# Performance work log

Hardware: AMD Instinct MI355X
Metric: run time of the kernel (lower is better)

Reference implementation:

```python
import jax, jax.numpy as jnp
import numpy as np

B, S, D, H = 2, 2048, 1024, 16
HD = D // H  # head_dim = 64


def setup_inputs() -> dict:
    key = jax.random.key(0)
    ks = jax.random.split(key, 10)
    sc = 1.0 / np.sqrt(D)
    x = jax.random.normal(ks[0], (B, S, D), dtype=jnp.float32)
    # causal mask, 0 = masked (module does masked_fill(mask == 0, -1e9))
    mask = jnp.broadcast_to(jnp.tril(jnp.ones((S, S), dtype=jnp.int32)), (B, S, S))
    return {
        "x": x,
        "mask": mask,
        "Wq": jax.random.normal(ks[1], (D, D), dtype=jnp.float32) * sc,
        "bq": jnp.zeros((D,), dtype=jnp.float32),
        "Wk": jax.random.normal(ks[2], (D, D), dtype=jnp.float32) * sc,
        "bk": jnp.zeros((D,), dtype=jnp.float32),
        "Wv": jax.random.normal(ks[3], (D, D), dtype=jnp.float32) * sc,
        "bv": jnp.zeros((D,), dtype=jnp.float32),
        "Wo": jax.random.normal(ks[4], (D, D), dtype=jnp.float32) * sc,
        "bo": jnp.zeros((D,), dtype=jnp.float32),
    }


def reference(x, mask, Wq, bq, Wk, bk, Wv, bv, Wo, bo):
    b, s, _ = x.shape
    # torch nn.Linear: y = x @ W.T + b
    def split_heads(t):
        return t.reshape(b, s, H, HD).transpose(0, 2, 1, 3)  # [B,H,S,hd]
    q = split_heads(x @ Wq.T + bq)
    k = split_heads(x @ Wk.T + bk)
    v = split_heads(x @ Wv.T + bv)
    scores = jnp.einsum("bhqd,bhkd->bhqk", q, k) / jnp.sqrt(jnp.float32(HD))
    scores = jnp.where(mask[:, None, :, :] == 0, jnp.float32(-1e9), scores)
    w = jax.nn.softmax(scores, axis=-1)
    out = jnp.einsum("bhqk,bhkd->bhqd", w, v)  # [B,H,S,hd]
    out = out.transpose(0, 2, 1, 3).reshape(b, s, D)
    return out @ Wo.T + bo
```

## Files before the change

kernel.cpp:

```cpp
#include <hip/hip_runtime.h>
#include <cstdint>


typedef __bf16 bf16x8 __attribute__((ext_vector_type(8)));
typedef float f32x4 __attribute__((ext_vector_type(4)));

__device__ inline f32x4 mfma16(bf16x8 a, bf16x8 b, f32x4 c) {
    return __builtin_amdgcn_mfma_f32_16x16x32_bf16(a, b, c, 0, 0, 0);
}

__device__ inline uint16_t f2bf(float f) {
    uint32_t u = __builtin_bit_cast(uint32_t, f);
    u += 0x7FFFu + ((u >> 16) & 1u);
    return (uint16_t)(u >> 16);
}

__device__ inline void gload_lds16(const uint16_t* g, uint16_t* l) {
    __builtin_amdgcn_global_load_lds(
        (const __attribute__((address_space(1))) uint32_t*)g,
        (__attribute__((address_space(3))) uint32_t*)l, 16, 0, 0);
}

__global__ __launch_bounds__(256) void cast_kernel(const float* __restrict__ src,
                                                   uint16_t* __restrict__ dst, int n4) {
    int i = blockIdx.x * 256 + threadIdx.x;
    if (i < n4) {
        float4 v = ((const float4*)src)[i];
        uint64_t p = (uint64_t)f2bf(v.x) | ((uint64_t)f2bf(v.y) << 16) |
                     ((uint64_t)f2bf(v.z) << 32) | ((uint64_t)f2bf(v.w) << 48);
        ((uint64_t*)dst)[i] = p;
    }
}

__global__ __launch_bounds__(256) void cast4_kernel(const float* __restrict__ a,
                                                    const float* __restrict__ b,
                                                    const float* __restrict__ c,
                                                    const float* __restrict__ d,
                                                    uint16_t* __restrict__ dst, int n4) {
    const float* srcs[4] = {a, b, c, d};
    const float* s = srcs[blockIdx.y];
    int i = blockIdx.x * 256 + threadIdx.x;
    if (i < n4) {
        float4 v = ((const float4*)s)[i];
        uint64_t p = (uint64_t)f2bf(v.x) | ((uint64_t)f2bf(v.y) << 16) |
                     ((uint64_t)f2bf(v.z) << 32) | ((uint64_t)f2bf(v.w) << 48);
        ((uint64_t*)(dst + (size_t)blockIdx.y * n4 * 4))[i] = p;
    }
}

template<int OUTF32>
__global__ __launch_bounds__(256) void gemm128(const uint16_t* __restrict__ A,
                                               const uint16_t* __restrict__ W,
                                               const float* __restrict__ b0,
                                               const float* __restrict__ b1,
                                               const float* __restrict__ b2,
                                               void* __restrict__ o0,
                                               void* __restrict__ o1,
                                               void* __restrict__ o2,
                                               int K, float s0, float s1, float s2) {
    __shared__ __align__(16) uint16_t Alds[2][128 * 32];
    __shared__ __align__(16) uint16_t Blds[2][128 * 32];
    const int tid = threadIdx.x;
    const int lane = tid & 63, w = tid >> 6;
    const int l16 = lane & 15, quad = lane >> 4;
    const int wm = w & 1, wn = w >> 1;
    const int m0 = blockIdx.x * 128, n0 = blockIdx.y * 128;

    f32x4 acc[4][4] = {};

    const int ci0 = w * 128 + lane;
    const uint16_t* ga0 = A + (size_t)(m0 + (ci0 >> 2)) * K + (ci0 & 3) * 8;
    const uint16_t* gb0 = W + (size_t)(n0 + (ci0 >> 2)) * K + (ci0 & 3) * 8;
    const int ci1 = ci0 + 64;
    const uint16_t* ga1 = A + (size_t)(m0 + (ci1 >> 2)) * K + (ci1 & 3) * 8;
    const uint16_t* gb1 = W + (size_t)(n0 + (ci1 >> 2)) * K + (ci1 & 3) * 8;

    gload_lds16(ga0, Alds[0] + (w * 2 + 0) * 512);
    gload_lds16(gb0, Blds[0] + (w * 2 + 0) * 512);
    gload_lds16(ga1, Alds[0] + (w * 2 + 1) * 512);
    gload_lds16(gb1, Blds[0] + (w * 2 + 1) * 512);

    const int niter = K >> 5;
    for (int i = 0; i < niter; ++i) {
        __syncthreads();
        if (i + 1 < niter) {
            const int k1 = (i + 1) << 5;
            uint16_t* Ad = Alds[(i + 1) & 1];
            uint16_t* Bd = Blds[(i + 1) & 1];
            gload_lds16(ga0 + k1, Ad + (w * 2 + 0) * 512);
            gload_lds16(gb0 + k1, Bd + (w * 2 + 0) * 512);
            gload_lds16(ga1 + k1, Ad + (w * 2 + 1) * 512);
            gload_lds16(gb1 + k1, Bd + (w * 2 + 1) * 512);
        }
        const uint16_t* Ab = Alds[i & 1];
        const uint16_t* Bb = Blds[i & 1];
        bf16x8 af[4], bw[4];
#pragma unroll
        for (int t = 0; t < 4; ++t) {
            af[t] = *(const bf16x8*)(Ab + (wm * 64 + t * 16 + l16) * 32 + quad * 8);
            bw[t] = *(const bf16x8*)(Bb + (wn * 64 + t * 16 + l16) * 32 + quad * 8);
        }
#pragma unroll
        for (int mt = 0; mt < 4; ++mt)
#pragma unroll
            for (int nt = 0; nt < 4; ++nt)
                acc[mt][nt] = mfma16(af[mt], bw[nt], acc[mt][nt]);
    }

#pragma unroll
    for (int nt = 0; nt < 4; ++nt) {
        int col = n0 + wn * 64 + nt * 16 + l16;
        int seg = col >> 10, lcol = col & 1023;
        const float* bp = (seg == 0) ? b0 : (seg == 1 ? b1 : b2);
        float scale    = (seg == 0) ? s0 : (seg == 1 ? s1 : s2);
        void* op       = (seg == 0) ? o0 : (seg == 1 ? o1 : o2);
        float bc = bp[lcol];
#pragma unroll
        for (int mt = 0; mt < 4; ++mt)
#pragma unroll
            for (int r = 0; r < 4; ++r) {
                int row = m0 + wm * 64 + mt * 16 + quad * 4 + r;
                float v = (acc[mt][nt][r] + bc) * scale;
                if (OUTF32) ((float*)op)[(size_t)row * 1024 + lcol] = v;
                else        ((uint16_t*)op)[(size_t)row * 1024 + lcol] = f2bf(v);
            }
    }
}

__global__ __launch_bounds__(256) void transpose_v(const uint16_t* __restrict__ V,
                                                   uint16_t* __restrict__ Vt) {
    __shared__ __align__(16) uint16_t T[64 * 72];
    const int s0 = blockIdx.x * 64;
    const int bh = blockIdx.y;
    const int b = bh >> 4, h = bh & 15;
    const int tid = threadIdx.x;
    const int r = tid >> 2, c = tid & 3;
#pragma unroll
    for (int half = 0; half < 2; ++half) {
        uint4 v = *(const uint4*)(V + (size_t)(b * 2048 + s0 + r) * 1024 + h * 64 + half * 32 + c * 8);
        *(uint4*)(T + r * 72 + half * 32 + c * 8) = v;
    }
    __syncthreads();
#pragma unroll
    for (int it = 0; it < 2; ++it) {
        int id = it * 256 + tid;
        int d = id >> 3, c8 = (id & 7) * 8;
        uint32_t wpk[4];
#pragma unroll
        for (int jj = 0; jj < 4; ++jj) {
            uint32_t lo = T[(c8 + 2 * jj) * 72 + d];
            uint32_t hi = T[(c8 + 2 * jj + 1) * 72 + d];
            wpk[jj] = lo | (hi << 16);
        }
        uint4 o; o.x = wpk[0]; o.y = wpk[1]; o.z = wpk[2]; o.w = wpk[3];
        *(uint4*)(Vt + ((size_t)bh * 64 + d) * 2048 + s0 + c8) = o;
    }
}

__global__ __launch_bounds__(256) void attn_kernel(const uint16_t* __restrict__ Q,
                                                   const uint16_t* __restrict__ K,
                                                   const uint16_t* __restrict__ Vt,
                                                   float* __restrict__ Oacc,
                                                   float* __restrict__ Lbuf) {
    const int S = 2048, D = 1024;
    __shared__ __align__(16) uint16_t Klds[64 * 72];
    __shared__ __align__(16) uint16_t Vlds[64 * 72];
    __shared__ __align__(16) uint16_t Plds[4 * 32 * 72];

    int x = 39 - (int)blockIdx.x;
    int g = (x >= 24) ? 3 : (x >= 12) ? 2 : (x >= 4) ? 1 : 0;
    int rem = x - 2 * g * (g + 1);
    int per = g + 1;
    int qb = 4 * g + rem / per;
    int chunk = rem % per;
    const int n_kb = 2 * qb + 2, kb_diag = 2 * qb;
    const int kb0 = chunk * 8;
    const int kb1 = (kb0 + 8 < n_kb) ? kb0 + 8 : n_kb;
    const int niter = kb1 - kb0;

    const int bh = blockIdx.y;
    const int b = bh >> 4, h = bh & 15;
    const int tid = threadIdx.x, lane = tid & 63, w = tid >> 6;
    const int l16 = lane & 15, quad = lane >> 4;
    const int q0 = qb * 128;
    const size_t baseQK = (size_t)b * S * D + h * 64;
    uint16_t* Pw = Plds + w * (32 * 72);

    bf16x8 aq[2][2];
#pragma unroll
    for (int mt = 0; mt < 2; ++mt)
#pragma unroll
        for (int c = 0; c < 2; ++c)
            aq[mt][c] = *(const bf16x8*)(Q + baseQK +
                (size_t)(q0 + w * 32 + mt * 16 + l16) * D + c * 32 + quad * 8);

    bf16x8 ones;
#pragma unroll
    for (int j = 0; j < 8; ++j) ones[j] = (__bf16)1.0f;

    f32x4 accO[2][4] = {};
    f32x4 accL[2] = {};

    const int srow = tid >> 2, scq = tid & 3;
    const uint16_t* Kg = K + baseQK + (size_t)srow * D + scq * 16;
    const uint16_t* Vg = Vt + ((size_t)bh * 64 + srow) * S + scq * 16;

    uint4 kA, kB, vA, vB;
    {
        const uint16_t* kg = Kg + (size_t)(kb0 * 64) * D;
        const uint16_t* vg = Vg + kb0 * 64;
        kA = *(const uint4*)kg; kB = *(const uint4*)(kg + 8);
        vA = *(const uint4*)vg; vB = *(const uint4*)(vg + 8);
    }

    for (int i = 0; i < niter; ++i) {
        const int kb = kb0 + i;
        if (i) __syncthreads();
        *(uint4*)(Klds + srow * 72 + scq * 16)     = kA;
        *(uint4*)(Klds + srow * 72 + scq * 16 + 8) = kB;
        *(uint4*)(Vlds + srow * 72 + scq * 16)     = vA;
        *(uint4*)(Vlds + srow * 72 + scq * 16 + 8) = vB;
        if (i + 1 < niter) {
            const uint16_t* kg = Kg + (size_t)((kb + 1) * 64) * D;
            const uint16_t* vg = Vg + (kb + 1) * 64;
            kA = *(const uint4*)kg; kB = *(const uint4*)(kg + 8);
            vA = *(const uint4*)vg; vB = *(const uint4*)(vg + 8);
        }
        __syncthreads();

        f32x4 sc[2][4];
#pragma unroll
        for (int t = 0; t < 4; ++t) {
            bf16x8 bk0 = *(const bf16x8*)(Klds + (t * 16 + l16) * 72 + quad * 8);
            bf16x8 bk1 = *(const bf16x8*)(Klds + (t * 16 + l16) * 72 + 32 + quad * 8);
            f32x4 z0 = {}; f32x4 z1 = {};
            sc[0][t] = mfma16(aq[0][1], bk1, mfma16(aq[0][0], bk0, z0));
            sc[1][t] = mfma16(aq[1][1], bk1, mfma16(aq[1][0], bk0, z1));
        }

        bf16x8 bv0[4], bv1[4];
#pragma unroll
        for (int nt = 0; nt < 4; ++nt) {
            bv0[nt] = *(const bf16x8*)(Vlds + (nt * 16 + l16) * 72 + quad * 8);
            bv1[nt] = *(const bf16x8*)(Vlds + (nt * 16 + l16) * 72 + 32 + quad * 8);
        }

        if (kb < kb_diag) {
#pragma unroll
            for (int mt = 0; mt < 2; ++mt)
#pragma unroll
                for (int r = 0; r < 4; ++r)
#pragma unroll
                    for (int t = 0; t < 4; ++t) {
                        float p = __builtin_amdgcn_exp2f(sc[mt][t][r]);
                        Pw[(mt * 16 + quad * 4 + r) * 72 + t * 16 + l16] =
                            (uint16_t)(__builtin_bit_cast(uint32_t, p) >> 16);
                    }
        } else {
#pragma unroll
            for (int mt = 0; mt < 2; ++mt)
#pragma unroll
                for (int r = 0; r < 4; ++r) {
                    const int qrow = q0 + w * 32 + mt * 16 + quad * 4 + r;
#pragma unroll
                    for (int t = 0; t < 4; ++t) {
                        float s = sc[mt][t][r];
                        int kcol = kb * 64 + t * 16 + l16;
                        if (kcol > qrow) s = -1e30f;
                        float p = __builtin_amdgcn_exp2f(s);
                        Pw[(mt * 16 + quad * 4 + r) * 72 + t * 16 + l16] =
                            (uint16_t)(__builtin_bit_cast(uint32_t, p) >> 16);
                    }
                }
        }

        __asm__ volatile("s_waitcnt lgkmcnt(0)" ::: "memory");

        bf16x8 ap0[2], ap1[2];
#pragma unroll
        for (int mt = 0; mt < 2; ++mt) {
            ap0[mt] = *(const bf16x8*)(Pw + (mt * 16 + l16) * 72 + quad * 8);
            ap1[mt] = *(const bf16x8*)(Pw + (mt * 16 + l16) * 72 + 32 + quad * 8);
        }
#pragma unroll
        for (int nt = 0; nt < 4; ++nt) {
            accO[0][nt] = mfma16(ap1[0], bv1[nt], mfma16(ap0[0], bv0[nt], accO[0][nt]));
            accO[1][nt] = mfma16(ap1[1], bv1[nt], mfma16(ap0[1], bv0[nt], accO[1][nt]));
        }
        accL[0] = mfma16(ap1[0], ones, mfma16(ap0[0], ones, accL[0]));
        accL[1] = mfma16(ap1[1], ones, mfma16(ap0[1], ones, accL[1]));
    }

#pragma unroll
    for (int mt = 0; mt < 2; ++mt)
#pragma unroll
        for (int r = 0; r < 4; ++r) {
            const int qrow = q0 + w * 32 + mt * 16 + quad * 4 + r;
            const size_t rh = (size_t)(b * S + qrow) * 16 + h;
            if (l16 == 0) atomicAdd(Lbuf + rh, accL[mt][r]);
            float* ob = Oacc + rh * 64 + l16;
#pragma unroll
            for (int nt = 0; nt < 4; ++nt)
                atomicAdd(ob + nt * 16, accO[mt][nt][r]);
        }
}

__global__ __launch_bounds__(256) void norm_kernel(const float* __restrict__ Oacc,
                                                   const float* __restrict__ Lbuf,
                                                   uint16_t* __restrict__ att) {
    int idx = blockIdx.x * 256 + threadIdx.x;
    float4 o = ((const float4*)Oacc)[idx];
    float inv = __builtin_amdgcn_rcpf(Lbuf[idx >> 4]);
    uint64_t p = (uint64_t)f2bf(o.x * inv) | ((uint64_t)f2bf(o.y * inv) << 16) |
                 ((uint64_t)f2bf(o.z * inv) << 32) | ((uint64_t)f2bf(o.w * inv) << 48);
    ((uint64_t*)att)[idx] = p;
}

extern "C" void kernel_launch(void* const* d_in, const int* in_sizes, int n_in,
                              void* d_out, int out_size, void* d_ws, size_t ws_size,
                              hipStream_t stream) {
    const float* x  = (const float*)d_in[0];
    const float* Wq = (const float*)d_in[2];
    const float* bq = (const float*)d_in[3];
    const float* Wk = (const float*)d_in[4];
    const float* bk = (const float*)d_in[5];
    const float* Wv = (const float*)d_in[6];
    const float* bv = (const float*)d_in[7];
    const float* Wo = (const float*)d_in[8];
    const float* bo = (const float*)d_in[9];
    float* out = (float*)d_out;

    const int B = 2, S = 2048, D = 1024, H = 16;
    const int M = B * S;

    uint8_t* w = (uint8_t*)d_ws;
    uint16_t* xbf  = (uint16_t*)(w);
    uint16_t* wqbf = (uint16_t*)(w + (size_t)( 8 << 20));
    uint16_t* qbf  = (uint16_t*)(w + (size_t)(16 << 20));
    uint16_t* kbf  = (uint16_t*)(w + (size_t)(24 << 20));
    uint16_t* vbf  = (uint16_t*)(w + (size_t)(32 << 20));
    uint16_t* vtbf = (uint16_t*)(w + (size_t)(40 << 20));
    float*    Oacc = (float*)(w + (size_t)(48 << 20));
    float*    Lbuf = (float*)(w + (size_t)(64 << 20));
    uint16_t* wobf = wqbf + (size_t)3 * D * D;
    uint16_t* attbf = xbf;

    int nx4 = M * D / 4;
    int nw4 = D * D / 4;
    cast_kernel<<<dim3((nx4 + 255) / 256), dim3(256), 0, stream>>>(x, xbf, nx4);
    cast4_kernel<<<dim3((nw4 + 255) / 256, 4), dim3(256), 0, stream>>>(
        Wq, Wk, Wv, Wo, wqbf, nw4);

    hipMemsetAsync(Oacc, 0, (size_t)M * D * sizeof(float) + (size_t)M * H * sizeof(float), stream);

    gemm128<0><<<dim3(M / 128, 3072 / 128), dim3(256), 0, stream>>>(
        xbf, wqbf, bq, bk, bv, qbf, kbf, vbf, D, 0.125f * 1.44269504f, 1.0f, 1.0f);

    transpose_v<<<dim3(S / 64, B * H), dim3(256), 0, stream>>>(vbf, vtbf);
    attn_kernel<<<dim3(40, B * H), dim3(256), 0, stream>>>(qbf, kbf, vtbf, Oacc, Lbuf);
    norm_kernel<<<dim3(M * D / 4 / 256), dim3(256), 0, stream>>>(Oacc, Lbuf, attbf);

    gemm128<1><<<dim3(M / 128, 1024 / 128), dim3(256), 0, stream>>>(
        attbf, wobf, bo, bo, bo, out, out, out, D, 1.0f, 1.0f, 1.0f);
}
```

Baseline: 235.1 us.

## Drop split-KV atomics and fuse softmax normalization into attention kernel

Each attention block now handles one full query block over all of its causal key blocks, instead of splitting the key range into chunks of up to 8 blocks. That removes the float atomics into Oacc and Lbuf, the memset that zeroed them, and the separate norm kernel. Normalization and the bf16 conversion happen in registers, and the result is written straight to the attention output buffer. The trade-off is a smaller grid (512 instead of 1280 blocks) with more uneven work per block: the last query block runs 32 iterations instead of at most 8. This may lengthen the attention kernel's critical path.

Measured after the change: 222.9 us. -5.2%, faster.

```diff
diff --git a/kernel.cpp b/kernel.cpp
--- a/kernel.cpp
+++ b/kernel.cpp
@@ -160,23 +160,14 @@
 __global__ __launch_bounds__(256) void attn_kernel(const uint16_t* __restrict__ Q,
                                                    const uint16_t* __restrict__ K,
                                                    const uint16_t* __restrict__ Vt,
-                                                   float* __restrict__ Oacc,
-                                                   float* __restrict__ Lbuf) {
+                                                   uint16_t* __restrict__ att) {
     const int S = 2048, D = 1024;
     __shared__ __align__(16) uint16_t Klds[64 * 72];
     __shared__ __align__(16) uint16_t Vlds[64 * 72];
     __shared__ __align__(16) uint16_t Plds[4 * 32 * 72];
 
-    int x = 39 - (int)blockIdx.x;
-    int g = (x >= 24) ? 3 : (x >= 12) ? 2 : (x >= 4) ? 1 : 0;
-    int rem = x - 2 * g * (g + 1);
-    int per = g + 1;
-    int qb = 4 * g + rem / per;
-    int chunk = rem % per;
-    const int n_kb = 2 * qb + 2, kb_diag = 2 * qb;
-    const int kb0 = chunk * 8;
-    const int kb1 = (kb0 + 8 < n_kb) ? kb0 + 8 : n_kb;
-    const int niter = kb1 - kb0;
+    const int qb = 15 - (int)blockIdx.x;
+    const int niter = 2 * qb + 2, kb_diag = 2 * qb;
 
     const int bh = blockIdx.y;
     const int b = bh >> 4, h = bh & 15;
@@ -206,21 +197,16 @@
     const uint16_t* Vg = Vt + ((size_t)bh * 64 + srow) * S + scq * 16;
 
     uint4 kA, kB, vA, vB;
-    {
-        const uint16_t* kg = Kg + (size_t)(kb0 * 64) * D;
-        const uint16_t* vg = Vg + kb0 * 64;
-        kA = *(const uint4*)kg; kB = *(const uint4*)(kg + 8);
-        vA = *(const uint4*)vg; vB = *(const uint4*)(vg + 8);
-    }
-
-    for (int i = 0; i < niter; ++i) {
-        const int kb = kb0 + i;
-        if (i) __syncthreads();
+    kA = *(const uint4*)Kg; kB = *(const uint4*)(Kg + 8);
+    vA = *(const uint4*)Vg; vB = *(const uint4*)(Vg + 8);
+
+    for (int kb = 0; kb < niter; ++kb) {
+        if (kb) __syncthreads();
         *(uint4*)(Klds + srow * 72 + scq * 16)     = kA;
         *(uint4*)(Klds + srow * 72 + scq * 16 + 8) = kB;
         *(uint4*)(Vlds + srow * 72 + scq * 16)     = vA;
         *(uint4*)(Vlds + srow * 72 + scq * 16 + 8) = vB;
-        if (i + 1 < niter) {
+        if (kb + 1 < niter) {
             const uint16_t* kg = Kg + (size_t)((kb + 1) * 64) * D;
             const uint16_t* vg = Vg + (kb + 1) * 64;
             kA = *(const uint4*)kg; kB = *(const uint4*)(kg + 8);
@@ -296,24 +282,12 @@
 #pragma unroll
         for (int r = 0; r < 4; ++r) {
             const int qrow = q0 + w * 32 + mt * 16 + quad * 4 + r;
-            const size_t rh = (size_t)(b * S + qrow) * 16 + h;
-            if (l16 == 0) atomicAdd(Lbuf + rh, accL[mt][r]);
-            float* ob = Oacc + rh * 64 + l16;
+            float inv = __builtin_amdgcn_rcpf(accL[mt][r]);
+            uint16_t* ob = att + (size_t)(b * S + qrow) * 1024 + h * 64 + l16;
 #pragma unroll
             for (int nt = 0; nt < 4; ++nt)
-                atomicAdd(ob + nt * 16, accO[mt][nt][r]);
-        }
-}
-
-__global__ __launch_bounds__(256) void norm_kernel(const float* __restrict__ Oacc,
-                                                   const float* __restrict__ Lbuf,
-                                                   uint16_t* __restrict__ att) {
-    int idx = blockIdx.x * 256 + threadIdx.x;
-    float4 o = ((const float4*)Oacc)[idx];
-    float inv = __builtin_amdgcn_rcpf(Lbuf[idx >> 4]);
-    uint64_t p = (uint64_t)f2bf(o.x * inv) | ((uint64_t)f2bf(o.y * inv) << 16) |
-                 ((uint64_t)f2bf(o.z * inv) << 32) | ((uint64_t)f2bf(o.w * inv) << 48);
-    ((uint64_t*)att)[idx] = p;
+                ob[nt * 16] = f2bf(accO[mt][nt][r] * inv);
+        }
 }
 
 extern "C" void kernel_launch(void* const* d_in, const int* in_sizes, int n_in,
@@ -340,8 +314,6 @@
     uint16_t* kbf  = (uint16_t*)(w + (size_t)(24 << 20));
     uint16_t* vbf  = (uint16_t*)(w + (size_t)(32 << 20));
     uint16_t* vtbf = (uint16_t*)(w + (size_t)(40 << 20));
-    float*    Oacc = (float*)(w + (size_t)(48 << 20));
-    float*    Lbuf = (float*)(w + (size_t)(64 << 20));
     uint16_t* wobf = wqbf + (size_t)3 * D * D;
     uint16_t* attbf = xbf;
 
@@ -351,14 +323,12 @@
     cast4_kernel<<<dim3((nw4 + 255) / 256, 4), dim3(256), 0, stream>>>(
         Wq, Wk, Wv, Wo, wqbf, nw4);
 
-    hipMemsetAsync(Oacc, 0, (size_t)M * D * sizeof(float) + (size_t)M * H * sizeof(float), stream);
-
     gemm128<0><<<dim3(M / 128, 3072 / 128), dim3(256), 0, stream>>>(
         xbf, wqbf, bq, bk, bv, qbf, kbf, vbf, D, 0.125f * 1.44269504f, 1.0f, 1.0f);
 
     transpose_v<<<dim3(S / 64, B * H), dim3(256), 0, stream>>>(vbf, vtbf);
-    attn_kernel<<<dim3(40, B * H), dim3(256), 0, stream>>>(qbf, kbf, vtbf, Oacc, Lbuf);
-    norm_kernel<<<dim3(M * D / 4 / 256), dim3(256), 0, stream>>>(Oacc, Lbuf, attbf);
+
+    attn_kernel<<<dim3(16, B * H), dim3(256), 0, stream>>>(qbf, kbf, vtbf, attbf);
 
     gemm128<1><<<dim3(M / 128, 1024 / 128), dim3(256), 0, stream>>>(
         attbf, wobf, bo, bo, bo, out, out, out, D, 1.0f, 1.0f, 1.0f);
```
